# Kernel tuning notes

Hardware: AMD Instinct MI355X
Metric: run time of the kernel (lower is better)

Reference implementation:

```python
import jax, jax.numpy as jnp
import numpy as np

B, S, D = 2, 2048, 512
H, HD = 8, 64  # num_heads, head_size; all_head_size = H*HD = 512


def setup_inputs() -> dict:
    key = jax.random.key(0)
    ks = jax.random.split(key, 11)
    sc = 0.02
    return {
        "query": jax.random.normal(ks[0], (B, S, D), jnp.float32),
        "key": jax.random.normal(ks[1], (B, S, D), jnp.float32),
        "value": jax.random.normal(ks[2], (B, S, D), jnp.float32),
        "Wq": jax.random.normal(ks[3], (D, H * HD), jnp.float32) * sc,
        "bq": jnp.zeros((H * HD,), jnp.float32),
        "Wk": jax.random.normal(ks[4], (D, H * HD), jnp.float32) * sc,
        "bk": jnp.zeros((H * HD,), jnp.float32),
        "Wv": jax.random.normal(ks[5], (D, H * HD), jnp.float32) * sc,
        "bv": jnp.zeros((H * HD,), jnp.float32),
        "Wo": jax.random.normal(ks[6], (H * HD, D), jnp.float32) * sc,
        "bo": jnp.zeros((D,), jnp.float32),
    }


def _split_heads(x):
    b, s, _ = x.shape
    return x.reshape(b, s, H, HD).transpose(0, 2, 1, 3)  # [B,H,S,HD]


def reference(query, key, value, Wq, bq, Wk, bk, Wv, bv, Wo, bo):
    q = _split_heads(query @ Wq + bq)
    k = _split_heads(key @ Wk + bk)
    v = _split_heads(value @ Wv + bv)
    scores = jnp.einsum("bhqd,bhkd->bhqk", q, k) / jnp.sqrt(jnp.asarray(HD, q.dtype))
    probs = jax.nn.softmax(scores, axis=-1)  # dropout rate 0.0, inference
    ctx = jnp.einsum("bhqk,bhkd->bhqd", probs, v)
    ctx = ctx.transpose(0, 2, 1, 3).reshape(query.shape[0], -1, H * HD)
    return ctx @ Wo + bo
```

## Files before the change

### kernel.cpp

```cpp
#include <hip/hip_runtime.h>
#include <math.h>

#define BATCH 2
#define SEQ 2048
#define DMODEL 512
#define NH 8
#define HDIM 64
#define MTOT (BATCH * SEQ)
#define QSIZE (BATCH * NH * SEQ * HDIM)
#define WSIZE (DMODEL * DMODEL)

typedef __attribute__((ext_vector_type(8))) short bf16x8;
typedef __attribute__((ext_vector_type(4))) float f32x4;

__device__ inline unsigned short f2bf(float f) {
    union { float f; unsigned u; } v; v.f = f;
    unsigned u = v.u;
    u += 0x7fffu + ((u >> 16) & 1u);
    return (unsigned short)(u >> 16);
}
__device__ inline unsigned pack2(float lo, float hi) {
    return (unsigned)f2bf(lo) | ((unsigned)f2bf(hi) << 16);
}

#define LSTR 72

#define WS_Q   ((size_t)0)
#define WS_K   ((size_t)QSIZE)
#define WS_V   (2 * (size_t)QSIZE)
#define WS_CTX (3 * (size_t)QSIZE)
#define WS_WT  (4 * (size_t)QSIZE)
#define WS_ABF (4 * (size_t)QSIZE + 4 * (size_t)WSIZE)

__global__ __launch_bounds__(256) void wt_prep_kernel(
    const float* __restrict__ Wq, const float* __restrict__ Wk,
    const float* __restrict__ Wv, const float* __restrict__ Wo,
    unsigned short* __restrict__ wt)
{
    const int z = blockIdx.z;
    const float* W = (z == 0) ? Wq : (z == 1) ? Wk : (z == 2) ? Wv : Wo;
    unsigned short* Wt = wt + (size_t)z * WSIZE;

    __shared__ float T[32][33];
    const int tid = threadIdx.x;
    const int k0 = blockIdx.x * 32, n0 = blockIdx.y * 32;

    {
        int r = tid >> 3, c = (tid & 7) * 4;
        float4 v = *(const float4*)&W[(size_t)(k0 + r) * DMODEL + n0 + c];
        T[r][c + 0] = v.x; T[r][c + 1] = v.y; T[r][c + 2] = v.z; T[r][c + 3] = v.w;
    }
    __syncthreads();
    {
        int n = tid >> 3, c = (tid & 7) * 4;
        uint2 o;
        o.x = pack2(T[c + 0][n], T[c + 1][n]);
        o.y = pack2(T[c + 2][n], T[c + 3][n]);
        *(uint2*)&Wt[(size_t)(n0 + n) * DMODEL + k0 + c] = o;
    }
}

__global__ __launch_bounds__(256) void inp_prep_kernel(
    const float* __restrict__ qin, const float* __restrict__ kin,
    const float* __restrict__ vin, unsigned short* __restrict__ abf)
{
    const int z = blockIdx.y;
    const float* src = (z == 0) ? qin : (z == 1) ? kin : vin;
    unsigned short* dst = abf + (size_t)z * QSIZE;

    const size_t i = ((size_t)blockIdx.x * 256 + threadIdx.x) * 8;
    float4 f0 = *(const float4*)(src + i);
    float4 f1 = *(const float4*)(src + i + 4);
    uint4 o;
    o.x = pack2(f0.x, f0.y); o.y = pack2(f0.z, f0.w);
    o.z = pack2(f1.x, f1.y); o.w = pack2(f1.z, f1.w);
    *(uint4*)(dst + i) = o;
}

__global__ __launch_bounds__(256) void qkv_mfma_kernel(
    unsigned short* __restrict__ ws,
    const float* __restrict__ bq, const float* __restrict__ bk,
    const float* __restrict__ bv)
{
    const int which = blockIdx.z;
    const unsigned short* A  = ws + WS_ABF + (size_t)which * QSIZE;
    const unsigned short* Wt = ws + WS_WT + (size_t)which * WSIZE;
    const float* bias = (which == 0) ? bq : (which == 1) ? bk : bv;
    unsigned short* out = ws + (size_t)which * QSIZE;

    __shared__ __align__(16) short As[128][LSTR];
    __shared__ __align__(16) short Bs[128][LSTR];

    const int tid = threadIdx.x;
    const int lane = tid & 63, wave = tid >> 6;
    const int lrow = lane & 15, quad = lane >> 4;
    const int m0 = blockIdx.y * 128, n0 = blockIdx.x * 128;

    const int sr = tid >> 1;
    const int sh = (tid & 1) * 32;

    f32x4 acc[2][8];
    #pragma unroll
    for (int i = 0; i < 2; ++i)
        #pragma unroll
        for (int n = 0; n < 8; ++n) acc[i][n] = f32x4{0.f, 0.f, 0.f, 0.f};

    for (int k0 = 0; k0 < DMODEL; k0 += 64) {
        __syncthreads();
        {
            const unsigned short* ap = A + (size_t)(m0 + sr) * DMODEL + k0 + sh;
            uint4 a0 = *(const uint4*)(ap + 0),  a1 = *(const uint4*)(ap + 8);
            uint4 a2 = *(const uint4*)(ap + 16), a3 = *(const uint4*)(ap + 24);
            *(uint4*)&As[sr][sh + 0]  = a0;
            *(uint4*)&As[sr][sh + 8]  = a1;
            *(uint4*)&As[sr][sh + 16] = a2;
            *(uint4*)&As[sr][sh + 24] = a3;
        }
        {
            const unsigned short* wp = Wt + (size_t)(n0 + sr) * DMODEL + k0 + sh;
            uint4 b0 = *(const uint4*)(wp + 0),  b1 = *(const uint4*)(wp + 8);
            uint4 b2 = *(const uint4*)(wp + 16), b3 = *(const uint4*)(wp + 24);
            *(uint4*)&Bs[sr][sh + 0]  = b0;
            *(uint4*)&Bs[sr][sh + 8]  = b1;
            *(uint4*)&Bs[sr][sh + 16] = b2;
            *(uint4*)&Bs[sr][sh + 24] = b3;
        }
        __syncthreads();
        #pragma unroll
        for (int s = 0; s < 2; ++s) {
            bf16x8 af[2];
            #pragma unroll
            for (int i = 0; i < 2; ++i)
                af[i] = *(const bf16x8*)&As[wave * 32 + i * 16 + lrow][s * 32 + quad * 8];
            #pragma unroll
            for (int n = 0; n < 8; ++n) {
                bf16x8 bf = *(const bf16x8*)&Bs[n * 16 + lrow][s * 32 + quad * 8];
                acc[0][n] = __builtin_amdgcn_mfma_f32_16x16x32_bf16(af[0], bf, acc[0][n], 0, 0, 0);
                acc[1][n] = __builtin_amdgcn_mfma_f32_16x16x32_bf16(af[1], bf, acc[1][n], 0, 0, 0);
            }
        }
    }

    if (which < 2) {
        const float scale = (which == 0) ? 0.125f : 1.0f;
        #pragma unroll
        for (int n = 0; n < 8; ++n) {
            const int col = n0 + n * 16 + lrow;
            const int h_ = col >> 6, hd_ = col & 63;
            const float bv_ = bias[col];
            #pragma unroll
            for (int i = 0; i < 2; ++i) {
                #pragma unroll
                for (int r = 0; r < 4; ++r) {
                    const int m = m0 + wave * 32 + i * 16 + quad * 4 + r;
                    const int b_ = m >> 11, s_ = m & (SEQ - 1);
                    const float v = (acc[i][n][r] + bv_) * scale;
                    out[((size_t)((b_ * NH + h_) * SEQ + s_)) * HDIM + hd_] = f2bf(v);
                }
            }
        }
    } else {
        #pragma unroll
        for (int n = 0; n < 8; ++n) {
            const int col = n0 + n * 16 + lrow;
            const int h_ = col >> 6, hd_ = col & 63;
            const float bv_ = bias[col];
            #pragma unroll
            for (int i = 0; i < 2; ++i) {
                const int m = m0 + wave * 32 + i * 16 + quad * 4;
                const int b_ = m >> 11, s_ = m & (SEQ - 1);
                uint2 o;
                o.x = pack2(acc[i][n][0] + bv_, acc[i][n][1] + bv_);
                o.y = pack2(acc[i][n][2] + bv_, acc[i][n][3] + bv_);
                *(uint2*)&out[((size_t)((b_ * NH + h_) * HDIM + hd_)) * SEQ + s_] = o;
            }
        }
    }
}

__global__ __launch_bounds__(256) void attn_mfma_kernel(
    const unsigned short* __restrict__ ws, unsigned short* __restrict__ ctx)
{
    const unsigned short* Q = ws + WS_Q;
    const unsigned short* K = ws + WS_K;
    const unsigned short* V = ws + WS_V;

    __shared__ __align__(16) short Ks[64][LSTR];
    __shared__ __align__(16) short Vt[64][LSTR];
    __shared__ __align__(16) short Ps[64][LSTR];

    const int bh = blockIdx.x;
    const int q0 = blockIdx.y * 64;
    const int tid = threadIdx.x;
    const int lane = tid & 63, wave = tid >> 6;
    const int lrow = lane & 15, quad = lane >> 4;
    const size_t base = (size_t)bh * SEQ * HDIM;

    const unsigned short* qrow = Q + base + (size_t)(q0 + wave * 16 + lrow) * HDIM;
    const bf16x8 qb0 = *(const bf16x8*)(qrow + quad * 8);
    const bf16x8 qb1 = *(const bf16x8*)(qrow + 32 + quad * 8);

    float m_prev = -1e30f, l_run = 0.f;
    f32x4 oacc[4];
    #pragma unroll
    for (int n = 0; n < 4; ++n) oacc[n] = f32x4{0.f, 0.f, 0.f, 0.f};

    const int kr = tid >> 2, kc = (tid & 3) * 16;
    const int vr = tid >> 2, vq = (tid & 3) * 16;

    for (int kt = 0; kt < SEQ; kt += 64) {
        __syncthreads();
        {
            const unsigned short* kp = K + base + (size_t)(kt + kr) * HDIM + kc;
            uint4 k0 = *(const uint4*)kp;
            uint4 k1 = *(const uint4*)(kp + 8);
            *(uint4*)&Ks[kr][kc]     = k0;
            *(uint4*)&Ks[kr][kc + 8] = k1;
        }
        {
            const unsigned short* vp = V + base + (size_t)vr * SEQ + kt + vq;
            uint4 v0 = *(const uint4*)vp;
            uint4 v1 = *(const uint4*)(vp + 8);
            *(uint4*)&Vt[vr][vq]     = v0;
            *(uint4*)&Vt[vr][vq + 8] = v1;
        }
        __syncthreads();

        f32x4 st[4];
        #pragma unroll
        for (int n = 0; n < 4; ++n) {
            bf16x8 ka0 = *(const bf16x8*)&Ks[n * 16 + lrow][quad * 8];
            bf16x8 ka1 = *(const bf16x8*)&Ks[n * 16 + lrow][32 + quad * 8];
            f32x4 z = f32x4{0.f, 0.f, 0.f, 0.f};
            z = __builtin_amdgcn_mfma_f32_16x16x32_bf16(ka0, qb0, z, 0, 0, 0);
            z = __builtin_amdgcn_mfma_f32_16x16x32_bf16(ka1, qb1, z, 0, 0, 0);
            st[n] = z;
        }

        float tmax = st[0][0];
        #pragma unroll
        for (int n = 0; n < 4; ++n)
            #pragma unroll
            for (int r = 0; r < 4; ++r) tmax = fmaxf(tmax, st[n][r]);
        tmax = fmaxf(tmax, __shfl_xor(tmax, 16));
        tmax = fmaxf(tmax, __shfl_xor(tmax, 32));

        const float mnew = fmaxf(m_prev, tmax);
        const float alpha = __expf(m_prev - mnew);
        float p[4][4];
        float tsum = 0.f;
        #pragma unroll
        for (int n = 0; n < 4; ++n)
            #pragma unroll
            for (int r = 0; r < 4; ++r) {
                p[n][r] = __expf(st[n][r] - mnew);
                tsum += p[n][r];
            }
        tsum += __shfl_xor(tsum, 16);
        tsum += __shfl_xor(tsum, 32);
        l_run = l_run * alpha + tsum;
        m_prev = mnew;
        #pragma unroll
        for (int n = 0; n < 4; ++n) {
            oacc[n][0] *= alpha; oacc[n][1] *= alpha;
            oacc[n][2] *= alpha; oacc[n][3] *= alpha;
        }
        #pragma unroll
        for (int n = 0; n < 4; ++n) {
            uint2 o;
            o.x = pack2(p[n][0], p[n][1]);
            o.y = pack2(p[n][2], p[n][3]);
            *(uint2*)&Ps[wave * 16 + lrow][n * 16 + quad * 4] = o;
        }

        bf16x8 pb0 = *(const bf16x8*)&Ps[wave * 16 + lrow][quad * 8];
        bf16x8 pb1 = *(const bf16x8*)&Ps[wave * 16 + lrow][32 + quad * 8];
        #pragma unroll
        for (int n = 0; n < 4; ++n) {
            bf16x8 va0 = *(const bf16x8*)&Vt[n * 16 + lrow][quad * 8];
            bf16x8 va1 = *(const bf16x8*)&Vt[n * 16 + lrow][32 + quad * 8];
            oacc[n] = __builtin_amdgcn_mfma_f32_16x16x32_bf16(va0, pb0, oacc[n], 0, 0, 0);
            oacc[n] = __builtin_amdgcn_mfma_f32_16x16x32_bf16(va1, pb1, oacc[n], 0, 0, 0);
        }
    }

    const int b_ = bh >> 3, h_ = bh & 7;
    const float inv = 1.f / l_run;
    const int qg = q0 + wave * 16 + lrow;
    unsigned short* crow = ctx + ((size_t)(b_ * SEQ + qg)) * DMODEL + h_ * HDIM;
    #pragma unroll
    for (int n = 0; n < 4; ++n) {
        uint2 o;
        o.x = pack2(oacc[n][0] * inv, oacc[n][1] * inv);
        o.y = pack2(oacc[n][2] * inv, oacc[n][3] * inv);
        *(uint2*)&crow[n * 16 + quad * 4] = o;
    }
}

__global__ __launch_bounds__(256) void out_proj_mfma_kernel(
    const unsigned short* __restrict__ ws, const float* __restrict__ bo,
    float* __restrict__ out)
{
    const unsigned short* ctx = ws + WS_CTX;
    const unsigned short* Wt  = ws + WS_WT + 3 * (size_t)WSIZE;

    __shared__ __align__(16) short As[128][LSTR];
    __shared__ __align__(16) short Bs[64][LSTR];

    const int tid = threadIdx.x;
    const int lane = tid & 63, wave = tid >> 6;
    const int lrow = lane & 15, quad = lane >> 4;
    const int m0 = blockIdx.y * 128, n0 = blockIdx.x * 64;

    const int sr = tid >> 1, sh = (tid & 1) * 32;
    const int br = tid >> 2, bqr = (tid & 3) * 16;

    f32x4 acc[2][4];
    #pragma unroll
    for (int i = 0; i < 2; ++i)
        #pragma unroll
        for (int n = 0; n < 4; ++n) acc[i][n] = f32x4{0.f, 0.f, 0.f, 0.f};

    for (int k0 = 0; k0 < DMODEL; k0 += 64) {
        __syncthreads();
        {
            const unsigned short* ap = ctx + (size_t)(m0 + sr) * DMODEL + k0 + sh;
            uint4 c0 = *(const uint4*)(ap + 0),  c1 = *(const uint4*)(ap + 8);
            uint4 c2 = *(const uint4*)(ap + 16), c3 = *(const uint4*)(ap + 24);
            *(uint4*)&As[sr][sh + 0]  = c0;
            *(uint4*)&As[sr][sh + 8]  = c1;
            *(uint4*)&As[sr][sh + 16] = c2;
            *(uint4*)&As[sr][sh + 24] = c3;
        }
        {
            const unsigned short* wp = Wt + (size_t)(n0 + br) * DMODEL + k0 + bqr;
            uint4 b0 = *(const uint4*)wp;
            uint4 b1 = *(const uint4*)(wp + 8);
            *(uint4*)&Bs[br][bqr]     = b0;
            *(uint4*)&Bs[br][bqr + 8] = b1;
        }
        __syncthreads();
        #pragma unroll
        for (int s = 0; s < 2; ++s) {
            bf16x8 af[2];
            #pragma unroll
            for (int i = 0; i < 2; ++i)
                af[i] = *(const bf16x8*)&As[wave * 32 + i * 16 + lrow][s * 32 + quad * 8];
            #pragma unroll
            for (int n = 0; n < 4; ++n) {
                bf16x8 bf = *(const bf16x8*)&Bs[n * 16 + lrow][s * 32 + quad * 8];
                acc[0][n] = __builtin_amdgcn_mfma_f32_16x16x32_bf16(af[0], bf, acc[0][n], 0, 0, 0);
                acc[1][n] = __builtin_amdgcn_mfma_f32_16x16x32_bf16(af[1], bf, acc[1][n], 0, 0, 0);
            }
        }
    }

    #pragma unroll
    for (int n = 0; n < 4; ++n) {
        const int col = n0 + n * 16 + lrow;
        const float bv_ = bo[col];
        #pragma unroll
        for (int i = 0; i < 2; ++i) {
            #pragma unroll
            for (int r = 0; r < 4; ++r) {
                const int m = m0 + wave * 32 + i * 16 + quad * 4 + r;
                out[(size_t)m * DMODEL + col] = acc[i][n][r] + bv_;
            }
        }
    }
}

extern "C" void kernel_launch(void* const* d_in, const int* in_sizes, int n_in,
                              void* d_out, int out_size, void* d_ws, size_t ws_size,
                              hipStream_t stream)
{
    const float* qin = (const float*)d_in[0];
    const float* kin = (const float*)d_in[1];
    const float* vin = (const float*)d_in[2];
    const float* Wq  = (const float*)d_in[3];
    const float* bq  = (const float*)d_in[4];
    const float* Wk  = (const float*)d_in[5];
    const float* bk  = (const float*)d_in[6];
    const float* Wv  = (const float*)d_in[7];
    const float* bv  = (const float*)d_in[8];
    const float* Wo  = (const float*)d_in[9];
    const float* bo  = (const float*)d_in[10];

    unsigned short* ws = (unsigned short*)d_ws;
    float* out = (float*)d_out;

    dim3 gw(DMODEL / 32, DMODEL / 32, 4);
    wt_prep_kernel<<<gw, 256, 0, stream>>>(Wq, Wk, Wv, Wo, ws + WS_WT);

    dim3 gi(QSIZE / (256 * 8), 3);
    inp_prep_kernel<<<gi, 256, 0, stream>>>(qin, kin, vin, ws + WS_ABF);

    dim3 gp(DMODEL / 128, MTOT / 128, 3);
    qkv_mfma_kernel<<<gp, 256, 0, stream>>>(ws, bq, bk, bv);

    dim3 ga(BATCH * NH, SEQ / 64);
    attn_mfma_kernel<<<ga, 256, 0, stream>>>(ws, ws + WS_CTX);

    dim3 go(DMODEL / 64, MTOT / 128);
    out_proj_mfma_kernel<<<go, 256, 0, stream>>>(ws, bo, out);
}
```

Baseline: 172.0 us.

## Prefetch tiles into registers, double query rows per attention block, transpose GEMM outputs

Adds register prefetching of the next K-tile of global loads in the QKV projection, attention and output projection kernels, so each tile's global loads overlap the current tile's MFMA work. The attention kernel now processes 128 queries per block (two 16-row groups per wave), reusing each K/V tile twice. The Q/K projection and the output projection swap MFMA operand roles so results come out transposed and can be stored as packed bf16x4 or float4 vectors. This costs more registers and halves the attention grid size, which may reduce occupancy.

```diff
diff --git a/kernel.cpp b/kernel.cpp
--- a/kernel.cpp
+++ b/kernel.cpp
@@ -96,8 +96,17 @@
     const int lrow = lane & 15, quad = lane >> 4;
     const int m0 = blockIdx.y * 128, n0 = blockIdx.x * 128;
 
-    const int sr = tid >> 1;
-    const int sh = (tid & 1) * 32;
+    const int sr = tid >> 1, sh = (tid & 1) * 32;
+
+    uint4 pa[4], pb[4];
+    {
+        const unsigned short* ap = A + (size_t)(m0 + sr) * DMODEL + sh;
+        pa[0] = *(const uint4*)ap;        pa[1] = *(const uint4*)(ap + 8);
+        pa[2] = *(const uint4*)(ap + 16); pa[3] = *(const uint4*)(ap + 24);
+        const unsigned short* wp = Wt + (size_t)(n0 + sr) * DMODEL + sh;
+        pb[0] = *(const uint4*)wp;        pb[1] = *(const uint4*)(wp + 8);
+        pb[2] = *(const uint4*)(wp + 16); pb[3] = *(const uint4*)(wp + 24);
+    }
 
     f32x4 acc[2][8];
     #pragma unroll
@@ -105,44 +114,63 @@
         #pragma unroll
         for (int n = 0; n < 8; ++n) acc[i][n] = f32x4{0.f, 0.f, 0.f, 0.f};
 
+    const bool tr = (which < 2);
+    const short (*At)[LSTR] = tr ? Bs : As;
+    const short (*Bt)[LSTR] = tr ? As : Bs;
+
     for (int k0 = 0; k0 < DMODEL; k0 += 64) {
         __syncthreads();
+        *(uint4*)&As[sr][sh]      = pa[0];
+        *(uint4*)&As[sr][sh + 8]  = pa[1];
+        *(uint4*)&As[sr][sh + 16] = pa[2];
+        *(uint4*)&As[sr][sh + 24] = pa[3];
+        *(uint4*)&Bs[sr][sh]      = pb[0];
+        *(uint4*)&Bs[sr][sh + 8]  = pb[1];
+        *(uint4*)&Bs[sr][sh + 16] = pb[2];
+        *(uint4*)&Bs[sr][sh + 24] = pb[3];
+        __syncthreads();
         {
-            const unsigned short* ap = A + (size_t)(m0 + sr) * DMODEL + k0 + sh;
-            uint4 a0 = *(const uint4*)(ap + 0),  a1 = *(const uint4*)(ap + 8);
-            uint4 a2 = *(const uint4*)(ap + 16), a3 = *(const uint4*)(ap + 24);
-            *(uint4*)&As[sr][sh + 0]  = a0;
-            *(uint4*)&As[sr][sh + 8]  = a1;
-            *(uint4*)&As[sr][sh + 16] = a2;
-            *(uint4*)&As[sr][sh + 24] = a3;
-        }
-        {
-            const unsigned short* wp = Wt + (size_t)(n0 + sr) * DMODEL + k0 + sh;
-            uint4 b0 = *(const uint4*)(wp + 0),  b1 = *(const uint4*)(wp + 8);
-            uint4 b2 = *(const uint4*)(wp + 16), b3 = *(const uint4*)(wp + 24);
-            *(uint4*)&Bs[sr][sh + 0]  = b0;
-            *(uint4*)&Bs[sr][sh + 8]  = b1;
-            *(uint4*)&Bs[sr][sh + 16] = b2;
-            *(uint4*)&Bs[sr][sh + 24] = b3;
-        }
-        __syncthreads();
+            const int k0n = (k0 + 64 < DMODEL) ? k0 + 64 : k0;
+            const unsigned short* ap = A + (size_t)(m0 + sr) * DMODEL + k0n + sh;
+            pa[0] = *(const uint4*)ap;        pa[1] = *(const uint4*)(ap + 8);
+            pa[2] = *(const uint4*)(ap + 16); pa[3] = *(const uint4*)(ap + 24);
+            const unsigned short* wp = Wt + (size_t)(n0 + sr) * DMODEL + k0n + sh;
+            pb[0] = *(const uint4*)wp;        pb[1] = *(const uint4*)(wp + 8);
+            pb[2] = *(const uint4*)(wp + 16); pb[3] = *(const uint4*)(wp + 24);
+        }
         #pragma unroll
         for (int s = 0; s < 2; ++s) {
             bf16x8 af[2];
             #pragma unroll
             for (int i = 0; i < 2; ++i)
-                af[i] = *(const bf16x8*)&As[wave * 32 + i * 16 + lrow][s * 32 + quad * 8];
+                af[i] = *(const bf16x8*)&At[wave * 32 + i * 16 + lrow][s * 32 + quad * 8];
             #pragma unroll
             for (int n = 0; n < 8; ++n) {
-                bf16x8 bf = *(const bf16x8*)&Bs[n * 16 + lrow][s * 32 + quad * 8];
+                bf16x8 bf = *(const bf16x8*)&Bt[n * 16 + lrow][s * 32 + quad * 8];
                 acc[0][n] = __builtin_amdgcn_mfma_f32_16x16x32_bf16(af[0], bf, acc[0][n], 0, 0, 0);
                 acc[1][n] = __builtin_amdgcn_mfma_f32_16x16x32_bf16(af[1], bf, acc[1][n], 0, 0, 0);
             }
         }
     }
 
-    if (which < 2) {
+    if (tr) {
         const float scale = (which == 0) ? 0.125f : 1.0f;
+        #pragma unroll
+        for (int i = 0; i < 2; ++i) {
+            const int dimb = n0 + wave * 32 + i * 16 + quad * 4;
+            const float4 b4 = *(const float4*)&bias[dimb];
+            const int h_ = dimb >> 6, hd_ = dimb & 63;
+            #pragma unroll
+            for (int n = 0; n < 8; ++n) {
+                const int tok = m0 + n * 16 + lrow;
+                const int b_ = tok >> 11, s_ = tok & (SEQ - 1);
+                uint2 o;
+                o.x = pack2((acc[i][n][0] + b4.x) * scale, (acc[i][n][1] + b4.y) * scale);
+                o.y = pack2((acc[i][n][2] + b4.z) * scale, (acc[i][n][3] + b4.w) * scale);
+                *(uint2*)&out[((size_t)((b_ * NH + h_) * SEQ + s_)) * HDIM + hd_] = o;
+            }
+        }
+    } else {
         #pragma unroll
         for (int n = 0; n < 8; ++n) {
             const int col = n0 + n * 16 + lrow;
@@ -150,25 +178,8 @@
             const float bv_ = bias[col];
             #pragma unroll
             for (int i = 0; i < 2; ++i) {
-                #pragma unroll
-                for (int r = 0; r < 4; ++r) {
-                    const int m = m0 + wave * 32 + i * 16 + quad * 4 + r;
-                    const int b_ = m >> 11, s_ = m & (SEQ - 1);
-                    const float v = (acc[i][n][r] + bv_) * scale;
-                    out[((size_t)((b_ * NH + h_) * SEQ + s_)) * HDIM + hd_] = f2bf(v);
-                }
-            }
-        }
-    } else {
-        #pragma unroll
-        for (int n = 0; n < 8; ++n) {
-            const int col = n0 + n * 16 + lrow;
-            const int h_ = col >> 6, hd_ = col & 63;
-            const float bv_ = bias[col];
-            #pragma unroll
-            for (int i = 0; i < 2; ++i) {
-                const int m = m0 + wave * 32 + i * 16 + quad * 4;
-                const int b_ = m >> 11, s_ = m & (SEQ - 1);
+                const int tok = m0 + wave * 32 + i * 16 + quad * 4;
+                const int b_ = tok >> 11, s_ = tok & (SEQ - 1);
                 uint2 o;
                 o.x = pack2(acc[i][n][0] + bv_, acc[i][n][1] + bv_);
                 o.y = pack2(acc[i][n][2] + bv_, acc[i][n][3] + bv_);
@@ -187,113 +198,141 @@
 
     __shared__ __align__(16) short Ks[64][LSTR];
     __shared__ __align__(16) short Vt[64][LSTR];
-    __shared__ __align__(16) short Ps[64][LSTR];
+    __shared__ __align__(16) short Ps[128][LSTR];
 
     const int bh = blockIdx.x;
-    const int q0 = blockIdx.y * 64;
+    const int q0 = blockIdx.y * 128;
     const int tid = threadIdx.x;
     const int lane = tid & 63, wave = tid >> 6;
     const int lrow = lane & 15, quad = lane >> 4;
     const size_t base = (size_t)bh * SEQ * HDIM;
 
-    const unsigned short* qrow = Q + base + (size_t)(q0 + wave * 16 + lrow) * HDIM;
-    const bf16x8 qb0 = *(const bf16x8*)(qrow + quad * 8);
-    const bf16x8 qb1 = *(const bf16x8*)(qrow + 32 + quad * 8);
-
-    float m_prev = -1e30f, l_run = 0.f;
-    f32x4 oacc[4];
-    #pragma unroll
-    for (int n = 0; n < 4; ++n) oacc[n] = f32x4{0.f, 0.f, 0.f, 0.f};
+    bf16x8 qb[2][2];
+    #pragma unroll
+    for (int j = 0; j < 2; ++j) {
+        const unsigned short* qr = Q + base + (size_t)(q0 + wave * 32 + j * 16 + lrow) * HDIM;
+        qb[j][0] = *(const bf16x8*)(qr + quad * 8);
+        qb[j][1] = *(const bf16x8*)(qr + 32 + quad * 8);
+    }
+
+    float m_prev[2] = {-1e30f, -1e30f}, l_run[2] = {0.f, 0.f};
+    f32x4 oacc[4][2];
+    #pragma unroll
+    for (int md = 0; md < 4; ++md)
+        #pragma unroll
+        for (int j = 0; j < 2; ++j) oacc[md][j] = f32x4{0.f, 0.f, 0.f, 0.f};
 
     const int kr = tid >> 2, kc = (tid & 3) * 16;
     const int vr = tid >> 2, vq = (tid & 3) * 16;
 
+    uint4 kpre[2], vpre[2];
+    {
+        const unsigned short* kp = K + base + (size_t)kr * HDIM + kc;
+        kpre[0] = *(const uint4*)kp;  kpre[1] = *(const uint4*)(kp + 8);
+        const unsigned short* vp = V + base + (size_t)vr * SEQ + vq;
+        vpre[0] = *(const uint4*)vp;  vpre[1] = *(const uint4*)(vp + 8);
+    }
+
     for (int kt = 0; kt < SEQ; kt += 64) {
         __syncthreads();
+        *(uint4*)&Ks[kr][kc]     = kpre[0];
+        *(uint4*)&Ks[kr][kc + 8] = kpre[1];
+        *(uint4*)&Vt[vr][vq]     = vpre[0];
+        *(uint4*)&Vt[vr][vq + 8] = vpre[1];
+        __syncthreads();
         {
-            const unsigned short* kp = K + base + (size_t)(kt + kr) * HDIM + kc;
-            uint4 k0 = *(const uint4*)kp;
-            uint4 k1 = *(const uint4*)(kp + 8);
-            *(uint4*)&Ks[kr][kc]     = k0;
-            *(uint4*)&Ks[kr][kc + 8] = k1;
-        }
-        {
-            const unsigned short* vp = V + base + (size_t)vr * SEQ + kt + vq;
-            uint4 v0 = *(const uint4*)vp;
-            uint4 v1 = *(const uint4*)(vp + 8);
-            *(uint4*)&Vt[vr][vq]     = v0;
-            *(uint4*)&Vt[vr][vq + 8] = v1;
-        }
-        __syncthreads();
-
-        f32x4 st[4];
-        #pragma unroll
-        for (int n = 0; n < 4; ++n) {
-            bf16x8 ka0 = *(const bf16x8*)&Ks[n * 16 + lrow][quad * 8];
-            bf16x8 ka1 = *(const bf16x8*)&Ks[n * 16 + lrow][32 + quad * 8];
-            f32x4 z = f32x4{0.f, 0.f, 0.f, 0.f};
-            z = __builtin_amdgcn_mfma_f32_16x16x32_bf16(ka0, qb0, z, 0, 0, 0);
-            z = __builtin_amdgcn_mfma_f32_16x16x32_bf16(ka1, qb1, z, 0, 0, 0);
-            st[n] = z;
-        }
-
-        float tmax = st[0][0];
-        #pragma unroll
-        for (int n = 0; n < 4; ++n)
-            #pragma unroll
-            for (int r = 0; r < 4; ++r) tmax = fmaxf(tmax, st[n][r]);
-        tmax = fmaxf(tmax, __shfl_xor(tmax, 16));
-        tmax = fmaxf(tmax, __shfl_xor(tmax, 32));
-
-        const float mnew = fmaxf(m_prev, tmax);
-        const float alpha = __expf(m_prev - mnew);
-        float p[4][4];
-        float tsum = 0.f;
-        #pragma unroll
-        for (int n = 0; n < 4; ++n)
-            #pragma unroll
-            for (int r = 0; r < 4; ++r) {
-                p[n][r] = __expf(st[n][r] - mnew);
-                tsum += p[n][r];
-            }
-        tsum += __shfl_xor(tsum, 16);
-        tsum += __shfl_xor(tsum, 32);
-        l_run = l_run * alpha + tsum;
-        m_prev = mnew;
-        #pragma unroll
-        for (int n = 0; n < 4; ++n) {
-            oacc[n][0] *= alpha; oacc[n][1] *= alpha;
-            oacc[n][2] *= alpha; oacc[n][3] *= alpha;
-        }
-        #pragma unroll
-        for (int n = 0; n < 4; ++n) {
+            const int ktn = (kt + 64 < SEQ) ? kt + 64 : kt;
+            const unsigned short* kp = K + base + (size_t)(ktn + kr) * HDIM + kc;
+            kpre[0] = *(const uint4*)kp;  kpre[1] = *(const uint4*)(kp + 8);
+            const unsigned short* vp = V + base + (size_t)vr * SEQ + ktn + vq;
+            vpre[0] = *(const uint4*)vp;  vpre[1] = *(const uint4*)(vp + 8);
+        }
+
+        f32x4 st[4][2];
+        #pragma unroll
+        for (int m = 0; m < 4; ++m) {
+            bf16x8 ka0 = *(const bf16x8*)&Ks[m * 16 + lrow][quad * 8];
+            bf16x8 ka1 = *(const bf16x8*)&Ks[m * 16 + lrow][32 + quad * 8];
+            #pragma unroll
+            for (int j = 0; j < 2; ++j) {
+                f32x4 z = f32x4{0.f, 0.f, 0.f, 0.f};
+                z = __builtin_amdgcn_mfma_f32_16x16x32_bf16(ka0, qb[j][0], z, 0, 0, 0);
+                z = __builtin_amdgcn_mfma_f32_16x16x32_bf16(ka1, qb[j][1], z, 0, 0, 0);
+                st[m][j] = z;
+            }
+        }
+
+        #pragma unroll
+        for (int j = 0; j < 2; ++j) {
+            float tmax = st[0][j][0];
+            #pragma unroll
+            for (int m = 0; m < 4; ++m)
+                #pragma unroll
+                for (int r = 0; r < 4; ++r) tmax = fmaxf(tmax, st[m][j][r]);
+            tmax = fmaxf(tmax, __shfl_xor(tmax, 16));
+            tmax = fmaxf(tmax, __shfl_xor(tmax, 32));
+
+            const float mnew = fmaxf(m_prev[j], tmax);
+            const float alpha = __expf(m_prev[j] - mnew);
+            float p[4][4];
+            float tsum = 0.f;
+            #pragma unroll
+            for (int m = 0; m < 4; ++m)
+                #pragma unroll
+                for (int r = 0; r < 4; ++r) {
+                    p[m][r] = __expf(st[m][j][r] - mnew);
+                    tsum += p[m][r];
+                }
+            tsum += __shfl_xor(tsum, 16);
+            tsum += __shfl_xor(tsum, 32);
+            l_run[j] = l_run[j] * alpha + tsum;
+            m_prev[j] = mnew;
+            #pragma unroll
+            for (int md = 0; md < 4; ++md) {
+                oacc[md][j][0] *= alpha; oacc[md][j][1] *= alpha;
+                oacc[md][j][2] *= alpha; oacc[md][j][3] *= alpha;
+            }
+            const int prow = wave * 32 + j * 16 + lrow;
+            #pragma unroll
+            for (int m = 0; m < 4; ++m) {
+                uint2 o;
+                o.x = pack2(p[m][0], p[m][1]);
+                o.y = pack2(p[m][2], p[m][3]);
+                *(uint2*)&Ps[prow][m * 16 + quad * 4] = o;
+            }
+        }
+
+        bf16x8 pb[2][2];
+        #pragma unroll
+        for (int j = 0; j < 2; ++j) {
+            pb[j][0] = *(const bf16x8*)&Ps[wave * 32 + j * 16 + lrow][quad * 8];
+            pb[j][1] = *(const bf16x8*)&Ps[wave * 32 + j * 16 + lrow][32 + quad * 8];
+        }
+        #pragma unroll
+        for (int md = 0; md < 4; ++md) {
+            bf16x8 va0 = *(const bf16x8*)&Vt[md * 16 + lrow][quad * 8];
+            bf16x8 va1 = *(const bf16x8*)&Vt[md * 16 + lrow][32 + quad * 8];
+            #pragma unroll
+            for (int j = 0; j < 2; ++j) {
+                oacc[md][j] = __builtin_amdgcn_mfma_f32_16x16x32_bf16(va0, pb[j][0], oacc[md][j], 0, 0, 0);
+                oacc[md][j] = __builtin_amdgcn_mfma_f32_16x16x32_bf16(va1, pb[j][1], oacc[md][j], 0, 0, 0);
+            }
+        }
+    }
+
+    const int b_ = bh >> 3, h_ = bh & 7;
+    #pragma unroll
+    for (int j = 0; j < 2; ++j) {
+        const float inv = 1.f / l_run[j];
+        const int qg = q0 + wave * 32 + j * 16 + lrow;
+        unsigned short* crow = ctx + ((size_t)(b_ * SEQ + qg)) * DMODEL + h_ * HDIM;
+        #pragma unroll
+        for (int md = 0; md < 4; ++md) {
             uint2 o;
-            o.x = pack2(p[n][0], p[n][1]);
-            o.y = pack2(p[n][2], p[n][3]);
-            *(uint2*)&Ps[wave * 16 + lrow][n * 16 + quad * 4] = o;
-        }
-
-        bf16x8 pb0 = *(const bf16x8*)&Ps[wave * 16 + lrow][quad * 8];
-        bf16x8 pb1 = *(const bf16x8*)&Ps[wave * 16 + lrow][32 + quad * 8];
-        #pragma unroll
-        for (int n = 0; n < 4; ++n) {
-            bf16x8 va0 = *(const bf16x8*)&Vt[n * 16 + lrow][quad * 8];
-            bf16x8 va1 = *(const bf16x8*)&Vt[n * 16 + lrow][32 + quad * 8];
-            oacc[n] = __builtin_amdgcn_mfma_f32_16x16x32_bf16(va0, pb0, oacc[n], 0, 0, 0);
-            oacc[n] = __builtin_amdgcn_mfma_f32_16x16x32_bf16(va1, pb1, oacc[n], 0, 0, 0);
-        }
-    }
-
-    const int b_ = bh >> 3, h_ = bh & 7;
-    const float inv = 1.f / l_run;
-    const int qg = q0 + wave * 16 + lrow;
-    unsigned short* crow = ctx + ((size_t)(b_ * SEQ + qg)) * DMODEL + h_ * HDIM;
-    #pragma unroll
-    for (int n = 0; n < 4; ++n) {
-        uint2 o;
-        o.x = pack2(oacc[n][0] * inv, oacc[n][1] * inv);
-        o.y = pack2(oacc[n][2] * inv, oacc[n][3] * inv);
-        *(uint2*)&crow[n * 16 + quad * 4] = o;
+            o.x = pack2(oacc[md][j][0] * inv, oacc[md][j][1] * inv);
+            o.y = pack2(oacc[md][j][2] * inv, oacc[md][j][3] * inv);
+            *(uint2*)&crow[md * 16 + quad * 4] = o;
+        }
     }
 }
 
@@ -304,16 +343,26 @@
     const unsigned short* ctx = ws + WS_CTX;
     const unsigned short* Wt  = ws + WS_WT + 3 * (size_t)WSIZE;
 
-    __shared__ __align__(16) short As[128][LSTR];
-    __shared__ __align__(16) short Bs[64][LSTR];
+    __shared__ __align__(16) short As[64][LSTR];
+    __shared__ __align__(16) short Bs[128][LSTR];
 
     const int tid = threadIdx.x;
     const int lane = tid & 63, wave = tid >> 6;
     const int lrow = lane & 15, quad = lane >> 4;
-    const int m0 = blockIdx.y * 128, n0 = blockIdx.x * 64;
-
-    const int sr = tid >> 1, sh = (tid & 1) * 32;
-    const int br = tid >> 2, bqr = (tid & 3) * 16;
+    const int m0 = blockIdx.y * 64, n0 = blockIdx.x * 128;
+
+    const int ar = tid >> 2, ac = (tid & 3) * 16;
+    const int br = tid >> 1, bc = (tid & 1) * 32;
+
+    uint4 pa0, pa1, pb[4];
+    {
+        const unsigned short* ap = ctx + (size_t)(m0 + ar) * DMODEL + ac;
+        pa0 = *(const uint4*)ap;
+        pa1 = *(const uint4*)(ap + 8);
+        const unsigned short* wp = Wt + (size_t)(n0 + br) * DMODEL + bc;
+        pb[0] = *(const uint4*)wp;        pb[1] = *(const uint4*)(wp + 8);
+        pb[2] = *(const uint4*)(wp + 16); pb[3] = *(const uint4*)(wp + 24);
+    }
 
     f32x4 acc[2][4];
     #pragma unroll
@@ -323,32 +372,31 @@
 
     for (int k0 = 0; k0 < DMODEL; k0 += 64) {
         __syncthreads();
+        *(uint4*)&As[ar][ac]      = pa0;
+        *(uint4*)&As[ar][ac + 8]  = pa1;
+        *(uint4*)&Bs[br][bc]      = pb[0];
+        *(uint4*)&Bs[br][bc + 8]  = pb[1];
+        *(uint4*)&Bs[br][bc + 16] = pb[2];
+        *(uint4*)&Bs[br][bc + 24] = pb[3];
+        __syncthreads();
         {
-            const unsigned short* ap = ctx + (size_t)(m0 + sr) * DMODEL + k0 + sh;
-            uint4 c0 = *(const uint4*)(ap + 0),  c1 = *(const uint4*)(ap + 8);
-            uint4 c2 = *(const uint4*)(ap + 16), c3 = *(const uint4*)(ap + 24);
-            *(uint4*)&As[sr][sh + 0]  = c0;
-            *(uint4*)&As[sr][sh + 8]  = c1;
-            *(uint4*)&As[sr][sh + 16] = c2;
-            *(uint4*)&As[sr][sh + 24] = c3;
-        }
-        {
-            const unsigned short* wp = Wt + (size_t)(n0 + br) * DMODEL + k0 + bqr;
-            uint4 b0 = *(const uint4*)wp;
-            uint4 b1 = *(const uint4*)(wp + 8);
-            *(uint4*)&Bs[br][bqr]     = b0;
-            *(uint4*)&Bs[br][bqr + 8] = b1;
-        }
-        __syncthreads();
+            const int k0n = (k0 + 64 < DMODEL) ? k0 + 64 : k0;
+            const unsigned short* ap = ctx + (size_t)(m0 + ar) * DMODEL + k0n + ac;
+            pa0 = *(const uint4*)ap;
+            pa1 = *(const uint4*)(ap + 8);
+            const unsigned short* wp = Wt + (size_t)(n0 + br) * DMODEL + k0n + bc;
+            pb[0] = *(const uint4*)wp;        pb[1] = *(const uint4*)(wp + 8);
+            pb[2] = *(const uint4*)(wp + 16); pb[3] = *(const uint4*)(wp + 24);
+        }
         #pragma unroll
         for (int s = 0; s < 2; ++s) {
             bf16x8 af[2];
             #pragma unroll
             for (int i = 0; i < 2; ++i)
-                af[i] = *(const bf16x8*)&As[wave * 32 + i * 16 + lrow][s * 32 + quad * 8];
+                af[i] = *(const bf16x8*)&Bs[wave * 32 + i * 16 + lrow][s * 32 + quad * 8];
             #pragma unroll
             for (int n = 0; n < 4; ++n) {
-                bf16x8 bf = *(const bf16x8*)&Bs[n * 16 + lrow][s * 32 + quad * 8];
+                bf16x8 bf = *(const bf16x8*)&As[n * 16 + lrow][s * 32 + quad * 8];
                 acc[0][n] = __builtin_amdgcn_mfma_f32_16x16x32_bf16(af[0], bf, acc[0][n], 0, 0, 0);
                 acc[1][n] = __builtin_amdgcn_mfma_f32_16x16x32_bf16(af[1], bf, acc[1][n], 0, 0, 0);
             }
@@ -356,16 +404,18 @@
     }
 
     #pragma unroll
-    for (int n = 0; n < 4; ++n) {
-        const int col = n0 + n * 16 + lrow;
-        const float bv_ = bo[col];
-        #pragma unroll
-        for (int i = 0; i < 2; ++i) {
-            #pragma unroll
-            for (int r = 0; r < 4; ++r) {
-                const int m = m0 + wave * 32 + i * 16 + quad * 4 + r;
-                out[(size_t)m * DMODEL + col] = acc[i][n][r] + bv_;
-            }
+    for (int i = 0; i < 2; ++i) {
+        const int dimb = n0 + wave * 32 + i * 16 + quad * 4;
+        const float4 b4 = *(const float4*)&bo[dimb];
+        #pragma unroll
+        for (int n = 0; n < 4; ++n) {
+            const int tok = m0 + n * 16 + lrow;
+            float4 o;
+            o.x = acc[i][n][0] + b4.x;
+            o.y = acc[i][n][1] + b4.y;
+            o.z = acc[i][n][2] + b4.z;
+            o.w = acc[i][n][3] + b4.w;
+            *(float4*)&out[(size_t)tok * DMODEL + dimb] = o;
         }
     }
 }
@@ -398,9 +448,9 @@
     dim3 gp(DMODEL / 128, MTOT / 128, 3);
     qkv_mfma_kernel<<<gp, 256, 0, stream>>>(ws, bq, bk, bv);
 
-    dim3 ga(BATCH * NH, SEQ / 64);
+    dim3 ga(BATCH * NH, SEQ / 128);
     attn_mfma_kernel<<<ga, 256, 0, stream>>>(ws, ws + WS_CTX);
 
-    dim3 go(DMODEL / 64, MTOT / 128);
+    dim3 go(DMODEL / 128, MTOT / 64);
     out_proj_mfma_kernel<<<go, 256, 0, stream>>>(ws, bo, out);
 }
```

Result: slower. 239.9 us (+39.5%).
